# Kernel optimization log

Measured on AMD Instinct MI355X. Metric: run time of the kernel, lower is better.

The kernel has to match this reference:

```python
import jax, jax.numpy as jnp
import numpy as np
import math

D = 1024
H = 16
HD = D // H

def layernorm(x, g, b, eps=1e-5):
    mu = jnp.mean(x, axis=-1, keepdims=True)
    var = jnp.var(x, axis=-1, keepdims=True)
    return (x - mu) * jax.lax.rsqrt(var + eps) * g + b

def setup_inputs() -> dict:
    key = jax.random.key(0)
    ks = jax.random.split(key, 12)
    s = 0.02
    return {
        "x": jax.random.normal(ks[0], (2, 2048, D), jnp.float32),
        "Wk": jax.random.normal(ks[1], (D, D), jnp.float32) * s,
        "Wq": jax.random.normal(ks[2], (D, D), jnp.float32) * s,
        "Wv": jax.random.normal(ks[3], (D, D), jnp.float32) * s,
        "Wp": jax.random.normal(ks[4], (D, D), jnp.float32) * s,
        "bp": jnp.zeros((D,), jnp.float32),
        "g1": jnp.ones((D,), jnp.float32),
        "b1": jnp.zeros((D,), jnp.float32),
        "g2": jnp.ones((D,), jnp.float32),
        "b2": jnp.zeros((D,), jnp.float32),
        "W1": jax.random.normal(ks[5], (D, 4 * D), jnp.float32) * s,
        "bm1": jnp.zeros((4 * D,), jnp.float32),
        "W2": jax.random.normal(ks[6], (4 * D, D), jnp.float32) * s,
        "bm2": jnp.zeros((D,), jnp.float32),
    }

def reference(x, Wk, Wq, Wv, Wp, bp, g1, b1, g2, b2, W1, bm1, W2, bm2):
    B, S, _ = x.shape
    xn = layernorm(x, g1, b1)  # pre-LN; residual uses xn (faithful to source)
    # project and split heads -> [B, H, S, HD]
    def heads(y):
        return y.reshape(B, S, H, HD).transpose(0, 2, 1, 3)
    q = heads(xn @ Wq)
    k = heads(xn @ Wk)
    v = heads(xn @ Wv)
    scale = 1.0 / math.sqrt(HD)
    att = jnp.einsum('bhsd,bhtd->bhst', q, k) * scale  # [B,H,S,S]
    diag = jnp.eye(S, dtype=bool)
    att = jnp.where(diag, -jnp.inf, att)  # exclude self-attention on diagonal
    att = jax.nn.softmax(att, axis=-1)
    y = jnp.einsum('bhst,bhtd->bhsd', att, v)
    y = y.transpose(0, 2, 1, 3).reshape(B, S, D)
    y = y @ Wp + bp  # dropout is identity at inference
    h = xn + y
    hn = layernorm(h, g2, b2)
    mlp = jax.nn.gelu(hn @ W1 + bm1, approximate=False) @ W2 + bm2
    return h + mlp
```

## Files before the change

### kernel.cpp

```cpp
#include <hip/hip_runtime.h>
#include <hip/hip_bf16.h>
#include <math.h>

#define BATCH   2
#define SEQ     2048
#define D_MODEL 1024
#define NHEAD   16
#define HEADD   64
#define NROWS   (BATCH * SEQ)
#define D_FF    4096
#define TPARTS  4
#define TSPAN   (SEQ / TPARTS)

typedef __bf16 bf16_t;
typedef __bf16 bf16x2 __attribute__((ext_vector_type(2)));
typedef __bf16 bf16x4 __attribute__((ext_vector_type(4)));
typedef __bf16 bf16x8 __attribute__((ext_vector_type(8)));
typedef float  f32x4  __attribute__((ext_vector_type(4)));

#define QSCALE 0.18033688011112042f

__device__ __forceinline__ void gload_lds16(const void* g, void* l) {
    __builtin_amdgcn_global_load_lds(
        (const __attribute__((address_space(1))) unsigned int*)g,
        (__attribute__((address_space(3))) unsigned int*)l, 16, 0, 0);
}

__global__ __launch_bounds__(256) void transpose_all6(
    const float* __restrict__ Wq, const float* __restrict__ Wk,
    const float* __restrict__ Wv, const float* __restrict__ Wp,
    const float* __restrict__ W1, const float* __restrict__ W2,
    bf16_t* __restrict__ Wqkvt, bf16_t* __restrict__ Wpt,
    bf16_t* __restrict__ W1t, bf16_t* __restrict__ W2t)
{
    __shared__ float tile[32][33];
    int bid = blockIdx.x;
    const float* W; bf16_t* Wt; int K, N, n0, k0;
    if (bid < 4096) {
        int seg = bid >> 10, t = bid & 1023;
        W  = (seg == 0) ? Wq : (seg == 1) ? Wk : (seg == 2) ? Wv : Wp;
        Wt = (seg < 3) ? (Wqkvt + (size_t)seg * 1024 * 1024) : Wpt;
        K = 1024; N = 1024;
        n0 = (t & 31) * 32; k0 = (t >> 5) * 32;
    } else if (bid < 8192) {
        int t = bid - 4096;
        W = W1; Wt = W1t; K = 1024; N = 4096;
        n0 = (t & 127) * 32; k0 = (t >> 7) * 32;
    } else {
        int t = bid - 8192;
        W = W2; Wt = W2t; K = 4096; N = 1024;
        n0 = (t & 31) * 32; k0 = (t >> 5) * 32;
    }
    int tx = threadIdx.x;
    int ty = threadIdx.y;
    #pragma unroll
    for (int i = 0; i < 32; i += 8)
        tile[ty + i][tx] = W[(size_t)(k0 + ty + i) * N + n0 + tx];
    __syncthreads();
    #pragma unroll
    for (int i = 0; i < 32; i += 8)
        Wt[(size_t)(n0 + ty + i) * K + k0 + tx] = (bf16_t)tile[tx][ty + i];
}

__global__ __launch_bounds__(256) void ln_kernel(
    const float* __restrict__ x, const float* __restrict__ g,
    const float* __restrict__ b, bf16_t* __restrict__ out)
{
    int row = blockIdx.x;
    int tid = threadIdx.x;
    const float* xr = x + (size_t)row * D_MODEL;
    f32x4 v = *(const f32x4*)(xr + tid * 4);
    float s  = v[0] + v[1] + v[2] + v[3];
    float s2 = v[0]*v[0] + v[1]*v[1] + v[2]*v[2] + v[3]*v[3];
    #pragma unroll
    for (int off = 32; off; off >>= 1) {
        s  += __shfl_down(s, off);
        s2 += __shfl_down(s2, off);
    }
    __shared__ float ps[4], ps2[4];
    int w = tid >> 6, lane = tid & 63;
    if (lane == 0) { ps[w] = s; ps2[w] = s2; }
    __syncthreads();
    float sum  = ps[0] + ps[1] + ps[2] + ps[3];
    float sum2 = ps2[0] + ps2[1] + ps2[2] + ps2[3];
    float mu  = sum * (1.0f / D_MODEL);
    float var = sum2 * (1.0f / D_MODEL) - mu * mu;
    float rs  = rsqrtf(var + 1e-5f);
    #pragma unroll
    for (int j = 0; j < 4; ++j) {
        int c = tid * 4 + j;
        out[(size_t)row * D_MODEL + c] = (bf16_t)((v[j] - mu) * rs * g[c] + b[c]);
    }
}

__global__ __launch_bounds__(512) void gemm256_gelu(
    const bf16_t* __restrict__ A, const bf16_t* __restrict__ Bt,
    const float* __restrict__ bias, bf16_t* __restrict__ out,
    int M, int N, int K)
{
    __shared__ bf16_t As[2][256 * 64];
    __shared__ bf16_t Bs[2][256 * 64];
    int tid = threadIdx.x;
    int bid = blockIdx.x;
    int m0 = (bid & 15) * 256;
    int n0 = (bid >> 4) * 256;
    int w = tid >> 6, lane = tid & 63, quad = lane >> 4, l15 = lane & 15;
    int wm = (w >> 2) * 128;
    int wn = (w & 3) * 64;
    int rxs = l15 & 7;

    int srow = tid >> 3;
    int sxor = (((tid & 7) ^ (srow & 7)) << 3);
    const bf16_t* Ap = A  + (size_t)(m0 + srow) * K + sxor;
    const bf16_t* Bp = Bt + (size_t)(n0 + srow) * K + sxor;

    f32x4 acc[8][4] = {};

    int nt = K >> 6;
    {
        bf16_t* AsW = &As[0][w * 512];
        bf16_t* BsW = &Bs[0][w * 512];
        #pragma unroll
        for (int h = 0; h < 2; ++h)
            #pragma unroll
            for (int p = 0; p < 2; ++p) {
                gload_lds16(Ap + (size_t)(h * 128 + p * 64) * K, AsW + h * 8192 + p * 4096);
                gload_lds16(Bp + (size_t)(h * 128 + p * 64) * K, BsW + h * 8192 + p * 4096);
            }
    }

    for (int t = 0; t < nt; ++t) {
        int cur = t & 1;
        const bf16_t* Asc = &As[cur][0];
        const bf16_t* Bsc = &Bs[cur][0];
        bf16_t* AsN = &As[cur ^ 1][w * 512];
        bf16_t* BsN = &Bs[cur ^ 1][w * 512];
        bool pf = (t + 1 < nt);
        int k1 = (t + 1) << 6;
        asm volatile("s_waitcnt vmcnt(0)" ::: "memory");
        __builtin_amdgcn_s_barrier();
        __builtin_amdgcn_sched_barrier(0);

        bf16x8 bfr[4][2];
        #pragma unroll
        for (int q = 0; q < 4; ++q) {
            bf16x8 af[2][2];
            #pragma unroll
            for (int ii = 0; ii < 2; ++ii)
                #pragma unroll
                for (int kk = 0; kk < 2; ++kk)
                    af[ii][kk] = *(const bf16x8*)&Asc[(wm + (2 * q + ii) * 16 + l15) * 64
                                                      + (((kk * 4 + quad) ^ rxs) << 3)];
            if (q == 0) {
                #pragma unroll
                for (int j = 0; j < 4; ++j)
                    #pragma unroll
                    for (int kk = 0; kk < 2; ++kk)
                        bfr[j][kk] = *(const bf16x8*)&Bsc[(wn + j * 16 + l15) * 64
                                                          + (((kk * 4 + quad) ^ rxs) << 3)];
            }
            if (q == 0 && pf) {
                #pragma unroll
                for (int h = 0; h < 2; ++h)
                    #pragma unroll
                    for (int p = 0; p < 2; ++p)
                        gload_lds16(Ap + (size_t)(h * 128 + p * 64) * K + k1,
                                    AsN + h * 8192 + p * 4096);
            }
            if (q == 1 && pf) {
                #pragma unroll
                for (int h = 0; h < 2; ++h)
                    #pragma unroll
                    for (int p = 0; p < 2; ++p)
                        gload_lds16(Bp + (size_t)(h * 128 + p * 64) * K + k1,
                                    BsN + h * 8192 + p * 4096);
            }
            #pragma unroll
            for (int ii = 0; ii < 2; ++ii)
                #pragma unroll
                for (int j = 0; j < 4; ++j)
                    #pragma unroll
                    for (int kk = 0; kk < 2; ++kk)
                        acc[2 * q + ii][j] = __builtin_amdgcn_mfma_f32_16x16x32_bf16(
                            af[ii][kk], bfr[j][kk], acc[2 * q + ii][j], 0, 0, 0);
        }
    }

    #pragma unroll
    for (int i = 0; i < 8; ++i)
    #pragma unroll
    for (int j = 0; j < 4; ++j) {
        int col  = n0 + wn + j * 16 + l15;
        int row0 = m0 + wm + i * 16 + quad * 4;
        float bv = bias[col];
        #pragma unroll
        for (int r = 0; r < 4; ++r) {
            int row = row0 + r;
            float u = acc[i][j][r] + bv;
            float y = u * (0.7978845608028654f + 0.03567740814f * u * u);
            float e = __builtin_amdgcn_exp2f(2.8853900817779268f * y);
            float r8 = __builtin_amdgcn_rcpf(e + 1.0f);
            out[(size_t)row * N + col] = (bf16_t)(u - u * r8);
        }
    }
}

template<int EPI, int BN>
__global__ __launch_bounds__(256) void gemm128(
    const bf16_t* __restrict__ A, const bf16_t* __restrict__ Bt,
    const float* __restrict__ bias, const void* __restrict__ resid,
    void* __restrict__ out, int M, int N, int K, int RY)
{
    constexpr int JN = BN / 32;
    constexpr int NBUF = (BN == 64) ? 3 : 2;
    __shared__ bf16_t As[NBUF][128 * 64];
    __shared__ bf16_t Bs[NBUF][BN * 64];
    int tid = threadIdx.x;
    int bid = blockIdx.x;
    int cx = bid & 3, cy = (bid >> 2) & 1, i0 = bid >> 3;
    int m0 = ((cx << 3) + (i0 & 7)) << 7;
    int n0 = (cy * RY + (i0 >> 3)) * BN;
    int w = tid >> 6, lane = tid & 63, quad = lane >> 4, l15 = lane & 15;
    int wm = (w & 1) * 64, wn = (w >> 1) * (BN / 2);
    int srow = tid >> 3;
    int sxor = (((tid & 7) ^ (srow & 7)) << 3);

    const bf16_t* Ap = A  + (size_t)(m0 + srow) * K + sxor;
    const bf16_t* Bp = Bt + (size_t)(n0 + srow) * K + sxor;

    int rxs = l15 & 7;

    auto stage = [&](int buf, int k0) {
        bf16_t* AsW = &As[buf][w * 512];
        bf16_t* BsW = &Bs[buf][w * 512];
        #pragma unroll
        for (int p = 0; p < 4; ++p)
            gload_lds16(Ap + (size_t)p * 32 * K + k0, AsW + p * 2048);
        #pragma unroll
        for (int p = 0; p < JN; ++p)
            gload_lds16(Bp + (size_t)p * 32 * K + k0, BsW + p * 2048);
    };

    f32x4 acc[4][JN] = {};

    int nt = K >> 6;
    stage(0, 0);
    if (NBUF == 3 && nt > 1) stage(1, 64);
    for (int t = 0; t < nt; ++t) {
        int cur = t % NBUF;
        if constexpr (NBUF == 3) {
            if (t + 2 < nt) {
                stage((t + 2) % NBUF, (t + 2) << 6);
                asm volatile("s_waitcnt vmcnt(12)" ::: "memory");
            } else if (t + 1 < nt) {
                asm volatile("s_waitcnt vmcnt(6)" ::: "memory");
            } else {
                asm volatile("s_waitcnt vmcnt(0)" ::: "memory");
            }
        } else {
            if (t + 1 < nt) {
                stage((t + 1) % NBUF, (t + 1) << 6);
                asm volatile("s_waitcnt vmcnt(8)" ::: "memory");
            } else {
                asm volatile("s_waitcnt vmcnt(0)" ::: "memory");
            }
        }
        __builtin_amdgcn_s_barrier();
        __builtin_amdgcn_sched_barrier(0);
        #pragma unroll
        for (int kk = 0; kk < 2; ++kk) {
            bf16x8 af[4], bfr[JN];
            #pragma unroll
            for (int i = 0; i < 4; ++i)
                af[i] = *(const bf16x8*)&As[cur][(wm + i * 16 + l15) * 64
                                            + ((((kk << 2) | quad) ^ rxs) << 3)];
            #pragma unroll
            for (int j = 0; j < JN; ++j)
                bfr[j] = *(const bf16x8*)&Bs[cur][(wn + j * 16 + l15) * 64
                                            + ((((kk << 2) | quad) ^ rxs) << 3)];
            #pragma unroll
            for (int i = 0; i < 4; ++i)
                #pragma unroll
                for (int j = 0; j < JN; ++j)
                    acc[i][j] = __builtin_amdgcn_mfma_f32_16x16x32_bf16(af[i], bfr[j], acc[i][j], 0, 0, 0);
        }
        __builtin_amdgcn_sched_barrier(0);
        asm volatile("s_waitcnt lgkmcnt(0)" ::: "memory");
        __builtin_amdgcn_s_barrier();
        __builtin_amdgcn_sched_barrier(0);
    }

    #pragma unroll
    for (int i = 0; i < 4; ++i)
    #pragma unroll
    for (int j = 0; j < JN; ++j) {
        int col  = n0 + wn + j * 16 + l15;
        int row0 = m0 + wm + i * 16 + quad * 4;
        if (EPI == 6) {
            int region = (n0 + wn + j * 16) >> 10;
            if (region < 2) {
                #pragma unroll
                for (int r = 0; r < 4; ++r) {
                    int row = row0 + r;
                    float v = acc[i][j][r];
                    if (region == 0) v *= QSCALE;
                    int b = row >> 11, s = row & 2047, hh = (col & 1023) >> 6, d = col & 63;
                    bf16_t* dst = (bf16_t*)out + (size_t)region * 4194304;
                    dst[(((size_t)(b * NHEAD + hh)) * SEQ + s) * HEADD + d] = (bf16_t)v;
                }
            } else {
                int dg = col - 2048, hh = dg >> 6, d = dg & 63;
                int b = row0 >> 11, s0 = row0 & 2047;
                bf16x4 pv;
                #pragma unroll
                for (int r = 0; r < 4; ++r) pv[r] = (bf16_t)acc[i][j][r];
                *(bf16x4*)((bf16_t*)out + 8388608
                           + (((size_t)(b * NHEAD + hh)) * HEADD + d) * SEQ + s0) = pv;
            }
        } else {
            float bv = bias[col];
            #pragma unroll
            for (int r = 0; r < 4; ++r) {
                int row = row0 + r;
                float vacc = acc[i][j][r] + bv;
                if (EPI == 1) {
                    float res = (float)((const bf16_t*)resid)[(size_t)row * N + col];
                    ((float*)out)[(size_t)row * N + col] = vacc + res;
                } else {
                    float res = ((const float*)resid)[(size_t)row * N + col];
                    ((float*)out)[(size_t)row * N + col] = vacc + res;
                }
            }
        }
    }
}

__global__ __launch_bounds__(256, 4) void attn_kernel(
    const bf16_t* __restrict__ q, const bf16_t* __restrict__ k,
    const bf16_t* __restrict__ vt, bf16_t* __restrict__ po,
    float* __restrict__ plsum)
{
    int gid = blockIdx.x;
    int xcd = gid & 7;
    int loc = gid >> 3;
    int bh  = xcd * 4 + (loc >> 6);
    int rest = loc & 63;
    int qt   = rest >> 2;
    int part = rest & 3;
    int tb0 = part * TSPAN, tend = tb0 + TSPAN;
    int b = bh >> 4, h = bh & 15;
    int tid = threadIdx.x, w = tid >> 6, lane = tid & 63;
    int quad = lane >> 4, l15 = lane & 15;
    int qbase = qt * 128 + w * 32;
    const bf16_t* qh = q  + (size_t)bh * SEQ * HEADD;
    const bf16_t* kh = k  + (size_t)bh * SEQ * HEADD;
    const bf16_t* vh = vt + (size_t)bh * HEADD * SEQ;

    bf16x8 qa[2][2];
    #pragma unroll
    for (int m = 0; m < 2; ++m)
        #pragma unroll
        for (int hf = 0; hf < 2; ++hf)
            qa[m][hf] = *(const bf16x8*)(qh + (size_t)(qbase + m * 16 + l15) * HEADD + hf * 32 + quad * 8);

    bf16x8 ones;
    #pragma unroll
    for (int j = 0; j < 8; ++j) ones[j] = (bf16_t)1.0f;

    __shared__ alignas(16) bf16_t Ks[32 * 72];
    __shared__ alignas(16) bf16_t Vs[64 * 40];
    __shared__ alignas(16) bf16_t Pl[4][32][40];

    int ksrow = tid >> 3, kscol = (tid & 7) * 8;
    int vsrow = tid >> 2, vscol = (tid & 3) * 8;
    const bf16_t* kg = kh + (size_t)ksrow * HEADD + kscol;
    const bf16_t* vg = vh + (size_t)vsrow * SEQ + vscol;

    f32x4 o[2][4] = {};
    f32x4 ls[2] = {};

    for (int t0 = tb0; t0 < tend; t0 += 32) {
        bf16x8 kreg = *(const bf16x8*)(kg + (size_t)t0 * HEADD);
        bf16x8 vreg = *(const bf16x8*)(vg + t0);
        __syncthreads();
        *(bf16x8*)&Ks[ksrow * 72 + kscol] = kreg;
        *(bf16x8*)&Vs[vsrow * 40 + vscol] = vreg;
        __syncthreads();

        bf16x8 kb[2][2], vf[4];
        #pragma unroll
        for (int jt = 0; jt < 2; ++jt)
            #pragma unroll
            for (int hf = 0; hf < 2; ++hf)
                kb[jt][hf] = *(const bf16x8*)&Ks[(2 * l15 + jt) * 72 + hf * 32 + quad * 8];
        #pragma unroll
        for (int dn = 0; dn < 4; ++dn)
            vf[dn] = *(const bf16x8*)&Vs[(dn * 16 + l15) * 40 + quad * 8];

        #pragma unroll
        for (int m = 0; m < 2; ++m) {
            f32x4 sc[2];
            #pragma unroll
            for (int jt = 0; jt < 2; ++jt) {
                f32x4 z = {};
                z = __builtin_amdgcn_mfma_f32_16x16x32_bf16(qa[m][0], kb[jt][0], z, 0, 0, 0);
                z = __builtin_amdgcn_mfma_f32_16x16x32_bf16(qa[m][1], kb[jt][1], z, 0, 0, 0);
                sc[jt] = z;
            }
            int qm = qbase + m * 16;
            bool dg = (t0 < qm + 16) && (t0 + 32 > qm);
            #pragma unroll
            for (int r = 0; r < 4; ++r) {
                int qrow = qm + quad * 4 + r;
                float p0 = __builtin_amdgcn_exp2f(sc[0][r]);
                float p1 = __builtin_amdgcn_exp2f(sc[1][r]);
                if (dg) {
                    int tg = t0 + 2 * l15;
                    if (tg == qrow)     p0 = 0.0f;
                    if (tg + 1 == qrow) p1 = 0.0f;
                }
                bf16x2 pp = { (bf16_t)p0, (bf16_t)p1 };
                *(bf16x2*)&Pl[w][m * 16 + quad * 4 + r][2 * l15] = pp;
            }
        }
        #pragma unroll
        for (int m = 0; m < 2; ++m) {
            bf16x8 pf = *(const bf16x8*)&Pl[w][m * 16 + l15][quad * 8];
            ls[m] = __builtin_amdgcn_mfma_f32_16x16x32_bf16(pf, ones, ls[m], 0, 0, 0);
            #pragma unroll
            for (int dn = 0; dn < 4; ++dn)
                o[m][dn] = __builtin_amdgcn_mfma_f32_16x16x32_bf16(pf, vf[dn], o[m][dn], 0, 0, 0);
        }
    }

    #pragma unroll
    for (int m = 0; m < 2; ++m)
        #pragma unroll
        for (int dn = 0; dn < 4; ++dn)
            #pragma unroll
            for (int r = 0; r < 4; ++r) {
                int qrow = qbase + m * 16 + quad * 4 + r;
                po[(((size_t)part * NROWS) + b * SEQ + qrow) * D_MODEL
                   + h * HEADD + dn * 16 + l15] = (bf16_t)o[m][dn][r];
            }
    if (l15 == 0) {
        #pragma unroll
        for (int m = 0; m < 2; ++m)
            #pragma unroll
            for (int r = 0; r < 4; ++r) {
                int qrow = qbase + m * 16 + quad * 4 + r;
                plsum[((size_t)part * 32 + bh) * SEQ + qrow] = ls[m][r];
            }
    }
}

__global__ __launch_bounds__(256) void attn_merge(
    const bf16_t* __restrict__ po, const float* __restrict__ plsum,
    bf16_t* __restrict__ y)
{
    int row = blockIdx.x;
    int tid = threadIdx.x;
    int c = tid * 4;
    int b = row >> 11, s = row & 2047;
    int bh = b * NHEAD + (c >> 6);
    float l = 0.0f;
    f32x4 ov = {};
    #pragma unroll
    for (int p = 0; p < TPARTS; ++p) {
        l += plsum[((size_t)p * 32 + bh) * SEQ + s];
        bf16x4 t = *(const bf16x4*)&po[((size_t)p * NROWS + row) * D_MODEL + c];
        #pragma unroll
        for (int j = 0; j < 4; ++j) ov[j] += (float)t[j];
    }
    float rl = 1.0f / l;
    bf16x4 out;
    #pragma unroll
    for (int j = 0; j < 4; ++j) out[j] = (bf16_t)(ov[j] * rl);
    *(bf16x4*)&y[(size_t)row * D_MODEL + c] = out;
}

extern "C" void kernel_launch(void* const* d_in, const int* in_sizes, int n_in,
                              void* d_out, int out_size, void* d_ws, size_t ws_size,
                              hipStream_t stream)
{
    const float* x   = (const float*)d_in[0];
    const float* Wk  = (const float*)d_in[1];
    const float* Wq  = (const float*)d_in[2];
    const float* Wv  = (const float*)d_in[3];
    const float* Wp  = (const float*)d_in[4];
    const float* bp  = (const float*)d_in[5];
    const float* g1  = (const float*)d_in[6];
    const float* b1  = (const float*)d_in[7];
    const float* g2  = (const float*)d_in[8];
    const float* b2  = (const float*)d_in[9];
    const float* W1  = (const float*)d_in[10];
    const float* bm1 = (const float*)d_in[11];
    const float* W2  = (const float*)d_in[12];
    const float* bm2 = (const float*)d_in[13];

    char* ws = (char*)d_ws;
    const size_t MB = 1024 * 1024;
    bf16_t* Wqkvt = (bf16_t*)(ws + 0 * MB);
    bf16_t* Wpt = (bf16_t*)(ws + 6 * MB);
    bf16_t* W1t = (bf16_t*)(ws + 8 * MB);
    bf16_t* W2t = (bf16_t*)(ws + 16 * MB);
    bf16_t* xn  = (bf16_t*)(ws + 24 * MB);
    bf16_t* qkv = (bf16_t*)(ws + 32 * MB);
    bf16_t* qb  = (bf16_t*)(ws + 32 * MB);
    bf16_t* kb  = (bf16_t*)(ws + 40 * MB);
    bf16_t* vtb = (bf16_t*)(ws + 48 * MB);
    bf16_t* yb  = (bf16_t*)(ws + 56 * MB);
    float*  hbuf= (float*) (ws + 64 * MB);
    bf16_t* po  = (bf16_t*)(ws + 64 * MB);
    float*  pls = (float*) (ws + 96 * MB);
    bf16_t* hn  = (bf16_t*)(ws + 24 * MB);
    bf16_t* act = (bf16_t*)(ws + 32 * MB);

    transpose_all6<<<12288, dim3(32, 8), 0, stream>>>(
        Wq, Wk, Wv, Wp, W1, W2, Wqkvt, Wpt, W1t, W2t);

    ln_kernel<<<NROWS, 256, 0, stream>>>(x, g1, b1, xn);

    gemm128<6, 128><<<768, 256, 0, stream>>>(xn, Wqkvt, nullptr, nullptr, qkv, NROWS, 3072, D_MODEL, 12);

    attn_kernel<<<2048, 256, 0, stream>>>(qb, kb, vtb, po, pls);
    attn_merge<<<NROWS, 256, 0, stream>>>(po, pls, yb);

    gemm128<1, 64><<<512, 256, 0, stream>>>(yb, Wpt, bp, xn, hbuf, NROWS, D_MODEL, D_MODEL, 8);

    ln_kernel<<<NROWS, 256, 0, stream>>>(hbuf, g2, b2, hn);

    gemm256_gelu<<<256, 512, 0, stream>>>(hn, W1t, bm1, act, NROWS, D_FF, D_MODEL);
    gemm128<3, 64><<<512, 256, 0, stream>>>(act, W2t, bm2, hbuf, d_out, NROWS, D_MODEL, D_FF, 8);
}
```

Baseline: 337.7 us.

## Run QKV projection on 256x256 GEMM tile and simplify 128x64 pipeline barriers

The QKV projection moves from the 128x128-tile GEMM to the 256x256-tile, 512-thread GEMM, which gains a templated epilogue for head-split Q/K/V writes alongside the GELU epilogue. The goal is higher operand reuse per block and fewer blocks (192 instead of 768). The 128x64 GEMM is specialised to BN=64 and now issues the prefetch of stage t+2 after the barrier. This removes the trailing lgkmcnt wait and second barrier per k-step. With only 192 blocks the QKV GEMM may underfill the GPU's compute units, and the reduced barrier scheme depends on the triple buffer to avoid LDS overwrite races.

Result: no change. 332.4 us (-1.6%).

```diff
diff --git a/kernel.cpp b/kernel.cpp
--- a/kernel.cpp
+++ b/kernel.cpp
@@ -93,9 +93,10 @@
     }
 }
 
-__global__ __launch_bounds__(512) void gemm256_gelu(
+template<int EPI>
+__global__ __launch_bounds__(512) void gemm256(
     const bf16_t* __restrict__ A, const bf16_t* __restrict__ Bt,
-    const float* __restrict__ bias, bf16_t* __restrict__ out,
+    const float* __restrict__ bias, void* __restrict__ out,
     int M, int N, int K)
 {
     __shared__ bf16_t As[2][256 * 64];
@@ -190,110 +191,6 @@
     for (int i = 0; i < 8; ++i)
     #pragma unroll
     for (int j = 0; j < 4; ++j) {
-        int col  = n0 + wn + j * 16 + l15;
-        int row0 = m0 + wm + i * 16 + quad * 4;
-        float bv = bias[col];
-        #pragma unroll
-        for (int r = 0; r < 4; ++r) {
-            int row = row0 + r;
-            float u = acc[i][j][r] + bv;
-            float y = u * (0.7978845608028654f + 0.03567740814f * u * u);
-            float e = __builtin_amdgcn_exp2f(2.8853900817779268f * y);
-            float r8 = __builtin_amdgcn_rcpf(e + 1.0f);
-            out[(size_t)row * N + col] = (bf16_t)(u - u * r8);
-        }
-    }
-}
-
-template<int EPI, int BN>
-__global__ __launch_bounds__(256) void gemm128(
-    const bf16_t* __restrict__ A, const bf16_t* __restrict__ Bt,
-    const float* __restrict__ bias, const void* __restrict__ resid,
-    void* __restrict__ out, int M, int N, int K, int RY)
-{
-    constexpr int JN = BN / 32;
-    constexpr int NBUF = (BN == 64) ? 3 : 2;
-    __shared__ bf16_t As[NBUF][128 * 64];
-    __shared__ bf16_t Bs[NBUF][BN * 64];
-    int tid = threadIdx.x;
-    int bid = blockIdx.x;
-    int cx = bid & 3, cy = (bid >> 2) & 1, i0 = bid >> 3;
-    int m0 = ((cx << 3) + (i0 & 7)) << 7;
-    int n0 = (cy * RY + (i0 >> 3)) * BN;
-    int w = tid >> 6, lane = tid & 63, quad = lane >> 4, l15 = lane & 15;
-    int wm = (w & 1) * 64, wn = (w >> 1) * (BN / 2);
-    int srow = tid >> 3;
-    int sxor = (((tid & 7) ^ (srow & 7)) << 3);
-
-    const bf16_t* Ap = A  + (size_t)(m0 + srow) * K + sxor;
-    const bf16_t* Bp = Bt + (size_t)(n0 + srow) * K + sxor;
-
-    int rxs = l15 & 7;
-
-    auto stage = [&](int buf, int k0) {
-        bf16_t* AsW = &As[buf][w * 512];
-        bf16_t* BsW = &Bs[buf][w * 512];
-        #pragma unroll
-        for (int p = 0; p < 4; ++p)
-            gload_lds16(Ap + (size_t)p * 32 * K + k0, AsW + p * 2048);
-        #pragma unroll
-        for (int p = 0; p < JN; ++p)
-            gload_lds16(Bp + (size_t)p * 32 * K + k0, BsW + p * 2048);
-    };
-
-    f32x4 acc[4][JN] = {};
-
-    int nt = K >> 6;
-    stage(0, 0);
-    if (NBUF == 3 && nt > 1) stage(1, 64);
-    for (int t = 0; t < nt; ++t) {
-        int cur = t % NBUF;
-        if constexpr (NBUF == 3) {
-            if (t + 2 < nt) {
-                stage((t + 2) % NBUF, (t + 2) << 6);
-                asm volatile("s_waitcnt vmcnt(12)" ::: "memory");
-            } else if (t + 1 < nt) {
-                asm volatile("s_waitcnt vmcnt(6)" ::: "memory");
-            } else {
-                asm volatile("s_waitcnt vmcnt(0)" ::: "memory");
-            }
-        } else {
-            if (t + 1 < nt) {
-                stage((t + 1) % NBUF, (t + 1) << 6);
-                asm volatile("s_waitcnt vmcnt(8)" ::: "memory");
-            } else {
-                asm volatile("s_waitcnt vmcnt(0)" ::: "memory");
-            }
-        }
-        __builtin_amdgcn_s_barrier();
-        __builtin_amdgcn_sched_barrier(0);
-        #pragma unroll
-        for (int kk = 0; kk < 2; ++kk) {
-            bf16x8 af[4], bfr[JN];
-            #pragma unroll
-            for (int i = 0; i < 4; ++i)
-                af[i] = *(const bf16x8*)&As[cur][(wm + i * 16 + l15) * 64
-                                            + ((((kk << 2) | quad) ^ rxs) << 3)];
-            #pragma unroll
-            for (int j = 0; j < JN; ++j)
-                bfr[j] = *(const bf16x8*)&Bs[cur][(wn + j * 16 + l15) * 64
-                                            + ((((kk << 2) | quad) ^ rxs) << 3)];
-            #pragma unroll
-            for (int i = 0; i < 4; ++i)
-                #pragma unroll
-                for (int j = 0; j < JN; ++j)
-                    acc[i][j] = __builtin_amdgcn_mfma_f32_16x16x32_bf16(af[i], bfr[j], acc[i][j], 0, 0, 0);
-        }
-        __builtin_amdgcn_sched_barrier(0);
-        asm volatile("s_waitcnt lgkmcnt(0)" ::: "memory");
-        __builtin_amdgcn_s_barrier();
-        __builtin_amdgcn_sched_barrier(0);
-    }
-
-    #pragma unroll
-    for (int i = 0; i < 4; ++i)
-    #pragma unroll
-    for (int j = 0; j < JN; ++j) {
         int col  = n0 + wn + j * 16 + l15;
         int row0 = m0 + wm + i * 16 + quad * 4;
         if (EPI == 6) {
@@ -322,14 +219,98 @@
             #pragma unroll
             for (int r = 0; r < 4; ++r) {
                 int row = row0 + r;
-                float vacc = acc[i][j][r] + bv;
-                if (EPI == 1) {
-                    float res = (float)((const bf16_t*)resid)[(size_t)row * N + col];
-                    ((float*)out)[(size_t)row * N + col] = vacc + res;
-                } else {
-                    float res = ((const float*)resid)[(size_t)row * N + col];
-                    ((float*)out)[(size_t)row * N + col] = vacc + res;
-                }
+                float u = acc[i][j][r] + bv;
+                float y = u * (0.7978845608028654f + 0.03567740814f * u * u);
+                float e = __builtin_amdgcn_exp2f(2.8853900817779268f * y);
+                float r8 = __builtin_amdgcn_rcpf(e + 1.0f);
+                ((bf16_t*)out)[(size_t)row * N + col] = (bf16_t)(u - u * r8);
+            }
+        }
+    }
+}
+
+template<int EPI>
+__global__ __launch_bounds__(256) void gemm128(
+    const bf16_t* __restrict__ A, const bf16_t* __restrict__ Bt,
+    const float* __restrict__ bias, const void* __restrict__ resid,
+    void* __restrict__ out, int M, int N, int K, int RY)
+{
+    __shared__ bf16_t As[3][128 * 64];
+    __shared__ bf16_t Bs[3][64 * 64];
+    int tid = threadIdx.x;
+    int bid = blockIdx.x;
+    int cx = bid & 3, cy = (bid >> 2) & 1, i0 = bid >> 3;
+    int m0 = ((cx << 3) + (i0 & 7)) << 7;
+    int n0 = (cy * RY + (i0 >> 3)) * 64;
+    int w = tid >> 6, lane = tid & 63, quad = lane >> 4, l15 = lane & 15;
+    int wm = (w & 1) * 64, wn = (w >> 1) * 32;
+    int srow = tid >> 3;
+    int sxor = (((tid & 7) ^ (srow & 7)) << 3);
+
+    const bf16_t* Ap = A  + (size_t)(m0 + srow) * K + sxor;
+    const bf16_t* Bp = Bt + (size_t)(n0 + srow) * K + sxor;
+
+    int rxs = l15 & 7;
+
+    auto stage = [&](int buf, int k0) {
+        bf16_t* AsW = &As[buf][w * 512];
+        bf16_t* BsW = &Bs[buf][w * 512];
+        #pragma unroll
+        for (int p = 0; p < 4; ++p)
+            gload_lds16(Ap + (size_t)p * 32 * K + k0, AsW + p * 2048);
+        #pragma unroll
+        for (int p = 0; p < 2; ++p)
+            gload_lds16(Bp + (size_t)p * 32 * K + k0, BsW + p * 2048);
+    };
+
+    f32x4 acc[4][2] = {};
+
+    int nt = K >> 6;
+    stage(0, 0);
+    if (nt > 1) stage(1, 64);
+    for (int t = 0; t < nt; ++t) {
+        int cur = t % 3;
+        if (t + 1 < nt) asm volatile("s_waitcnt vmcnt(6)" ::: "memory");
+        else            asm volatile("s_waitcnt vmcnt(0)" ::: "memory");
+        __builtin_amdgcn_s_barrier();
+        __builtin_amdgcn_sched_barrier(0);
+        if (t + 2 < nt) stage((t + 2) % 3, (t + 2) << 6);
+        #pragma unroll
+        for (int kk = 0; kk < 2; ++kk) {
+            bf16x8 af[4], bfr[2];
+            #pragma unroll
+            for (int i = 0; i < 4; ++i)
+                af[i] = *(const bf16x8*)&As[cur][(wm + i * 16 + l15) * 64
+                                            + ((((kk << 2) | quad) ^ rxs) << 3)];
+            #pragma unroll
+            for (int j = 0; j < 2; ++j)
+                bfr[j] = *(const bf16x8*)&Bs[cur][(wn + j * 16 + l15) * 64
+                                            + ((((kk << 2) | quad) ^ rxs) << 3)];
+            #pragma unroll
+            for (int i = 0; i < 4; ++i)
+                #pragma unroll
+                for (int j = 0; j < 2; ++j)
+                    acc[i][j] = __builtin_amdgcn_mfma_f32_16x16x32_bf16(af[i], bfr[j], acc[i][j], 0, 0, 0);
+        }
+    }
+
+    #pragma unroll
+    for (int i = 0; i < 4; ++i)
+    #pragma unroll
+    for (int j = 0; j < 2; ++j) {
+        int col  = n0 + wn + j * 16 + l15;
+        int row0 = m0 + wm + i * 16 + quad * 4;
+        float bv = bias[col];
+        #pragma unroll
+        for (int r = 0; r < 4; ++r) {
+            int row = row0 + r;
+            float vacc = acc[i][j][r] + bv;
+            if (EPI == 1) {
+                float res = (float)((const bf16_t*)resid)[(size_t)row * N + col];
+                ((float*)out)[(size_t)row * N + col] = vacc + res;
+            } else {
+                float res = ((const float*)resid)[(size_t)row * N + col];
+                ((float*)out)[(size_t)row * N + col] = vacc + res;
             }
         }
     }
@@ -521,15 +502,15 @@
 
     ln_kernel<<<NROWS, 256, 0, stream>>>(x, g1, b1, xn);
 
-    gemm128<6, 128><<<768, 256, 0, stream>>>(xn, Wqkvt, nullptr, nullptr, qkv, NROWS, 3072, D_MODEL, 12);
+    gemm256<6><<<192, 512, 0, stream>>>(xn, Wqkvt, nullptr, qkv, NROWS, 3072, D_MODEL);
 
     attn_kernel<<<2048, 256, 0, stream>>>(qb, kb, vtb, po, pls);
     attn_merge<<<NROWS, 256, 0, stream>>>(po, pls, yb);
 
-    gemm128<1, 64><<<512, 256, 0, stream>>>(yb, Wpt, bp, xn, hbuf, NROWS, D_MODEL, D_MODEL, 8);
+    gemm128<1><<<512, 256, 0, stream>>>(yb, Wpt, bp, xn, hbuf, NROWS, D_MODEL, D_MODEL, 8);
 
     ln_kernel<<<NROWS, 256, 0, stream>>>(hbuf, g2, b2, hn);
 
-    gemm256_gelu<<<256, 512, 0, stream>>>(hn, W1t, bm1, act, NROWS, D_FF, D_MODEL);
-    gemm128<3, 64><<<512, 256, 0, stream>>>(act, W2t, bm2, hbuf, d_out, NROWS, D_MODEL, D_FF, 8);
-}
+    gemm256<2><<<256, 512, 0, stream>>>(hn, W1t, bm1, act, NROWS, D_FF, D_MODEL);
+    gemm128<3><<<512, 256, 0, stream>>>(act, W2t, bm2, hbuf, d_out, NROWS, D_MODEL, D_FF, 8);
+}
```
